# Kernel tuning notes

Hardware: AMD Instinct MI355X
Metric: run time of the kernel (lower is better)

The kernel has to match this reference:

```python
import jax, jax.numpy as jnp
import numpy as np

# Segment geometry (from init_kwargs): modes ['u','uv','v'] -> out_v = alpha * x_u @ W_uv
U = 128
V = 128
IN_OFF = [0, 128, 256, 384]
W_OFF = [k * U * V for k in range(8)]          # [0,16384,...,114688]
OUT_OFF = [0, 128, 256, 384]
IN_STRIDE = 512
OUT_STRIDE = 512
W_STRIDE = 8 * U * V                           # 131072
# (in_seg, w_seg, out_seg, coefficient)
PATHS = [(0, 0, 0, 1.0), (1, 1, 1, 1.0), (2, 2, 2, 1.0), (3, 3, 3, 1.0),
         (0, 4, 1, 0.5), (1, 5, 2, 0.5), (2, 6, 3, 0.5), (3, 7, 0, 0.5)]
B = 32768
E = 4  # num_embeddings (experts)


def setup_inputs() -> dict:
    key = jax.random.key(0)
    k1, k2, k3 = jax.random.split(key, 3)
    tensor_in = jax.random.normal(k1, (B, IN_STRIDE), dtype=jnp.float32)
    tensor_w = jax.random.normal(k2, (E, W_STRIDE), dtype=jnp.float32)
    tensor_w_id = jax.random.randint(k3, (B,), 0, E, dtype=jnp.int32)
    return {"tensor_in": tensor_in, "tensor_w": tensor_w, "tensor_w_id": tensor_w_id}


def _batch_linear(tensor_in, tensor_w, tensor_w_id):
    """Segmented path-indexed grouped linear (cuEquivariance BatchLinear fwd).

    tensor_in: [B, IN_STRIDE]; tensor_w: [E, W_STRIDE]; tensor_w_id: [B] int in [0,E).
    For each path (i, j, k, alpha):
        out[b, OUT_OFF[k]:+V] += alpha * x[b, IN_OFF[i]:+U] @ W[w_id[b], seg j].reshape(U, V)
    """
    nb = tensor_in.shape[0]
    ne = tensor_w.shape[0]
    onehot = jax.nn.one_hot(tensor_w_id, ne, dtype=tensor_in.dtype)  # [B, E]
    out = jnp.zeros((nb, OUT_STRIDE), dtype=tensor_in.dtype)
    for (i, j, k, a) in PATHS:
        x = tensor_in[:, IN_OFF[i]:IN_OFF[i] + U]                    # [B, U]
        w_seg = tensor_w[:, W_OFF[j]:W_OFF[j] + U * V].reshape(ne, U, V)
        # masked per-expert dense GEMMs (small fixed expert count)
        y = jnp.zeros((nb, V), dtype=tensor_in.dtype)
        for e in range(ne):
            y = y + onehot[:, e:e + 1] * (x @ w_seg[e])              # [B, V]
        out = out.at[:, OUT_OFF[k]:OUT_OFF[k] + V].add(a * y)
    return out


def reference(tensor_in, tensor_w, tensor_w_id):
    return _batch_linear(tensor_in, tensor_w, tensor_w_id)
```

## Files before the change

### kernel.cpp

```cpp
#include <hip/hip_runtime.h>
#include <stdint.h>

#define U 128
#define V 128
#define IN_STRIDE 512
#define OUT_STRIDE 512
#define W_STRIDE (8 * U * V)
#define NB 32768
#define NE 4

#define WS_WSHUF 0
#define WS_CNT   1048576
#define WS_SORT  1048640

typedef __bf16 bf16x8 __attribute__((ext_vector_type(8)));
typedef float f32x16 __attribute__((ext_vector_type(16)));
typedef unsigned int u32x4 __attribute__((ext_vector_type(4)));

static __device__ __forceinline__ unsigned short f2bf(float f) {
    unsigned int u = __builtin_bit_cast(unsigned int, f);
    u += 0x7FFFu + ((u >> 16) & 1u);
    return (unsigned short)(u >> 16);
}

__global__ void prep_kernel(const float* __restrict__ w, unsigned short* __restrict__ wshuf,
                            unsigned int* __restrict__ cnt) {
    if (blockIdx.x == 0 && threadIdx.x < NE) cnt[threadIdx.x] = 0u;
    int t = blockIdx.x * 256 + threadIdx.x;
    int lane = t & 63;
    int kt = (t >> 6) & 7;
    int nt = (t >> 9) & 3;
    int s  = (t >> 11) & 7;
    int e  = (t >> 14) & 3;
    int kbase = kt * 16 + ((lane >> 5) << 3);
    int n = nt * 32 + (lane & 31);
    const float* src = w + (size_t)e * W_STRIDE + (size_t)s * (U * V) + n;
    float sc = (s >= 4) ? 0.5f : 1.0f;
    __attribute__((aligned(16))) unsigned short o[8];
#pragma unroll
    for (int j = 0; j < 8; j++) o[j] = f2bf(src[(size_t)(kbase + j) * V] * sc);
    *(u32x4*)(wshuf + (size_t)t * 8) = *(const u32x4*)o;
}

__global__ void scatter_kernel(const int* __restrict__ wid, unsigned int* __restrict__ cnt,
                               int* __restrict__ sorted) {
    __shared__ unsigned int lcnt[NE];
    __shared__ unsigned int lbase[NE];
    int t = threadIdx.x;
    if (t < NE) lcnt[t] = 0u;
    __syncthreads();
    int i = blockIdx.x * 256 + t;
    int e = wid[i];
    unsigned int lpos = atomicAdd(&lcnt[e], 1u);
    __syncthreads();
    if (t < NE) lbase[t] = atomicAdd(&cnt[t], lcnt[t]);
    __syncthreads();
    sorted[e * NB + (int)(lbase[e] + lpos)] = i;
}

__global__ __launch_bounds__(512, 4) void gemm_kernel(
        const float* __restrict__ x, const unsigned short* __restrict__ wshuf,
        const unsigned int* __restrict__ cnt, const int* __restrict__ sorted,
        float* __restrict__ out) {
    const int rowbase = blockIdx.x * 32;
    __shared__ float ldsf[32][512];
    __shared__ int rowid[32];

    const unsigned int p1 = cnt[0];
    const unsigned int p2 = p1 + cnt[1];
    const unsigned int p3 = p2 + cnt[2];

    const int t = threadIdx.x;
    const int w = t >> 6, lane = t & 63;
    const int l5 = lane >> 5, m0 = lane & 31;
    const int kout = w >> 1, nhalf = w & 1;

    int rid[4];
#pragma unroll
    for (int i = 0; i < 4; i++) {
        unsigned int ls = (unsigned int)(rowbase + 4 * w + i);
        int e = (ls >= p1) + (ls >= p2) + (ls >= p3);
        unsigned int pe = (e == 0) ? 0u : (e == 1) ? p1 : (e == 2) ? p2 : p3;
        rid[i] = sorted[e * NB + (int)(ls - pe)];
    }
    if (t < 32) {
        unsigned int ls = (unsigned int)(rowbase + t);
        int e = (ls >= p1) + (ls >= p2) + (ls >= p3);
        unsigned int pe = (e == 0) ? 0u : (e == 1) ? p1 : (e == 2) ? p2 : p3;
        rowid[t] = sorted[e * NB + (int)(ls - pe)];
    }

#pragma unroll
    for (int i = 0; i < 4; i++) {
        int r = 4 * w + i;
        int rs = r & 7;
        const float* xb = x + (size_t)rid[i] * IN_STRIDE + ((m0 ^ rs) << 2) + l5 * 128;
#pragma unroll
        for (int h = 0; h < 2; h++) {
            __builtin_amdgcn_global_load_lds(
                (const __attribute__((address_space(1))) unsigned int*)(xb + h * 256),
                (__attribute__((address_space(3))) unsigned int*)&ldsf[r][h * 256],
                16, 0, 0);
        }
    }

    const unsigned int lh = (unsigned int)rowbase, lt = (unsigned int)(rowbase + 31);
    const int ehead = (lh >= p1) + (lh >= p2) + (lh >= p3);
    const int etail = (lt >= p1) + (lt >= p2) + (lt >= p3);
    const unsigned int l0 = (unsigned int)(rowbase + m0);
    const int e0 = (l0 >= p1) + (l0 >= p2) + (l0 >= p3);

    const int xbc1 = (kout + 3) & 3;
    const int xbs[2] = {kout, xbc1};
    const int sgs[2] = {kout, xbc1 + 4};
    const int rsw = m0 & 7;

    f32x16 acc0 = {}, acc1 = {};

    if (ehead == etail) {
        const unsigned short* wb0 =
            wshuf + (size_t)(((ehead * 8 + sgs[0]) * 4 + nhalf * 2) * 8) * 512 + (size_t)lane * 8;
        u32x4 bp[8];
#pragma unroll
        for (int kt = 0; kt < 4; kt++) {
            bp[kt * 2]     = *(const u32x4*)(wb0 + (size_t)kt * 512);
            bp[kt * 2 + 1] = *(const u32x4*)(wb0 + (size_t)(8 + kt) * 512);
        }
        __syncthreads();

#pragma unroll
        for (int c = 0; c < 2; c++) {
            const float* ar = &ldsf[m0][xbs[c] * 128];
            const unsigned short* wb =
                wshuf + (size_t)(((ehead * 8 + sgs[c]) * 4 + nhalf * 2) * 8) * 512 + (size_t)lane * 8;
#pragma unroll
            for (int kt = 0; kt < 8; kt++) {
                int gj0 = kt * 4 + l5 * 2;
                float4 va = *(const float4*)(ar + ((gj0 ^ rsw) << 2));
                float4 vb = *(const float4*)(ar + (((gj0 + 1) ^ rsw) << 2));
                bf16x8 a;
                a[0] = (__bf16)va.x; a[1] = (__bf16)va.y;
                a[2] = (__bf16)va.z; a[3] = (__bf16)va.w;
                a[4] = (__bf16)vb.x; a[5] = (__bf16)vb.y;
                a[6] = (__bf16)vb.z; a[7] = (__bf16)vb.w;
                bf16x8 b0, b1;
                if (c == 0 && kt < 4) {
                    b0 = __builtin_bit_cast(bf16x8, bp[kt * 2]);
                    b1 = __builtin_bit_cast(bf16x8, bp[kt * 2 + 1]);
                } else {
                    b0 = __builtin_bit_cast(bf16x8, *(const u32x4*)(wb + (size_t)kt * 512));
                    b1 = __builtin_bit_cast(bf16x8, *(const u32x4*)(wb + (size_t)(8 + kt) * 512));
                }
                acc0 = __builtin_amdgcn_mfma_f32_32x32x16_bf16(a, b0, acc0, 0, 0, 0);
                acc1 = __builtin_amdgcn_mfma_f32_32x32x16_bf16(a, b1, acc1, 0, 0, 0);
            }
        }
    } else {
        unsigned int msk[4];
#pragma unroll
        for (int e = 0; e < 4; e++) msk[e] = (e0 == e) ? 0xFFFFFFFFu : 0u;
        __syncthreads();
#pragma unroll
        for (int c = 0; c < 2; c++) {
            const float* ar = &ldsf[m0][xbs[c] * 128];
#pragma unroll
            for (int kt = 0; kt < 8; kt++) {
                int gj0 = kt * 4 + l5 * 2;
                float4 va = *(const float4*)(ar + ((gj0 ^ rsw) << 2));
                float4 vb = *(const float4*)(ar + (((gj0 + 1) ^ rsw) << 2));
                __attribute__((aligned(16))) unsigned short au[8];
                au[0] = f2bf(va.x); au[1] = f2bf(va.y);
                au[2] = f2bf(va.z); au[3] = f2bf(va.w);
                au[4] = f2bf(vb.x); au[5] = f2bf(vb.y);
                au[6] = f2bf(vb.z); au[7] = f2bf(vb.w);
                u32x4 araw = *(const u32x4*)au;
#pragma unroll
                for (int e = 0; e < 4; e++) {
                    u32x4 mm = {msk[e], msk[e], msk[e], msk[e]};
                    bf16x8 am = __builtin_bit_cast(bf16x8, araw & mm);
                    const unsigned short* wb =
                        wshuf + (size_t)(((e * 8 + sgs[c]) * 4 + nhalf * 2) * 8) * 512 + (size_t)lane * 8;
                    bf16x8 b0 = __builtin_bit_cast(bf16x8, *(const u32x4*)(wb + (size_t)kt * 512));
                    bf16x8 b1 = __builtin_bit_cast(bf16x8, *(const u32x4*)(wb + (size_t)(8 + kt) * 512));
                    acc0 = __builtin_amdgcn_mfma_f32_32x32x16_bf16(am, b0, acc0, 0, 0, 0);
                    acc1 = __builtin_amdgcn_mfma_f32_32x32x16_bf16(am, b1, acc1, 0, 0, 0);
                }
            }
        }
    }

    const int colb = kout * 128 + nhalf * 64 + m0;
    const int rh = l5 << 2;
#pragma unroll
    for (int q = 0; q < 4; q++) {
#pragma unroll
        for (int d = 0; d < 4; d++) {
            int reg = q * 4 + d;
            int rl = d + 8 * q + rh;
            float* o = out + (size_t)rowid[rl] * OUT_STRIDE + colb;
            o[0]  = acc0[reg];
            o[32] = acc1[reg];
        }
    }
}

extern "C" void kernel_launch(void* const* d_in, const int* in_sizes, int n_in,
                              void* d_out, int out_size, void* d_ws, size_t ws_size,
                              hipStream_t stream) {
    const float* x = (const float*)d_in[0];
    const float* w = (const float*)d_in[1];
    const int* wid = (const int*)d_in[2];
    float* out = (float*)d_out;

    unsigned short* wshuf = (unsigned short*)((char*)d_ws + WS_WSHUF);
    unsigned int* cnt = (unsigned int*)((char*)d_ws + WS_CNT);
    int* sorted = (int*)((char*)d_ws + WS_SORT);

    prep_kernel<<<256, 256, 0, stream>>>(w, wshuf, cnt);
    scatter_kernel<<<128, 256, 0, stream>>>(wid, cnt, sorted);
    gemm_kernel<<<1024, 512, 0, stream>>>(x, wshuf, cnt, sorted, out);
}
```

Measured before the change: 136.7 us.

## Make GEMM blocks persistent over four row tiles with double-buffered X and register-resident weights

Result: slower. 198.3 us (+45.0%).

```diff
diff --git a/kernel.cpp b/kernel.cpp
--- a/kernel.cpp
+++ b/kernel.cpp
@@ -8,6 +8,7 @@
 #define W_STRIDE (8 * U * V)
 #define NB 32768
 #define NE 4
+#define NT 4
 
 #define WS_WSHUF 0
 #define WS_CNT   1048576
@@ -58,13 +59,13 @@
     sorted[e * NB + (int)(lbase[e] + lpos)] = i;
 }
 
-__global__ __launch_bounds__(512, 4) void gemm_kernel(
+__global__ __launch_bounds__(512, 2) void gemm_kernel(
         const float* __restrict__ x, const unsigned short* __restrict__ wshuf,
         const unsigned int* __restrict__ cnt, const int* __restrict__ sorted,
         float* __restrict__ out) {
-    const int rowbase = blockIdx.x * 32;
-    __shared__ float ldsf[32][512];
-    __shared__ int rowid[32];
+    const int blk = blockIdx.x;
+    __shared__ float ldsf[2][32][512];
+    __shared__ int rowid[128];
 
     const unsigned int p1 = cnt[0];
     const unsigned int p2 = p1 + cnt[1];
@@ -74,134 +75,179 @@
     const int w = t >> 6, lane = t & 63;
     const int l5 = lane >> 5, m0 = lane & 31;
     const int kout = w >> 1, nhalf = w & 1;
-
-    int rid[4];
-#pragma unroll
-    for (int i = 0; i < 4; i++) {
-        unsigned int ls = (unsigned int)(rowbase + 4 * w + i);
-        int e = (ls >= p1) + (ls >= p2) + (ls >= p3);
-        unsigned int pe = (e == 0) ? 0u : (e == 1) ? p1 : (e == 2) ? p2 : p3;
-        rid[i] = sorted[e * NB + (int)(ls - pe)];
+    const int rsw = m0 & 7;
+    const int xb1 = (kout + 3) & 3;
+
+#define EXPERT_OF(ls) (((ls) >= p1) + ((ls) >= p2) + ((ls) >= p3))
+#define PREFIX_OF(e)  ((e) == 0 ? 0u : (e) == 1 ? p1 : (e) == 2 ? p2 : p3)
+
+    if (t < 128) {
+        unsigned int ls = (unsigned int)(blk * 128 + t);
+        int e = EXPERT_OF(ls);
+        rowid[t] = sorted[e * NB + (int)(ls - PREFIX_OF(e))];
     }
-    if (t < 32) {
-        unsigned int ls = (unsigned int)(rowbase + t);
-        int e = (ls >= p1) + (ls >= p2) + (ls >= p3);
-        unsigned int pe = (e == 0) ? 0u : (e == 1) ? p1 : (e == 2) ? p2 : p3;
-        rowid[t] = sorted[e * NB + (int)(ls - pe)];
-    }
+
+    u32x4 bp[32];
+
+#define LOADB(eu) do { \
+    _Pragma("unroll") \
+    for (int c_ = 0; c_ < 2; c_++) { \
+        const int sg_ = c_ ? (xb1 + 4) : kout; \
+        const unsigned short* wb_ = wshuf + \
+            (size_t)((((eu) * 8 + sg_) * 4 + nhalf * 2) * 8) * 512 + (size_t)lane * 8; \
+        _Pragma("unroll") \
+        for (int kt_ = 0; kt_ < 8; kt_++) { \
+            bp[c_ * 16 + kt_ * 2]     = *(const u32x4*)(wb_ + (size_t)kt_ * 512); \
+            bp[c_ * 16 + kt_ * 2 + 1] = *(const u32x4*)(wb_ + (size_t)(8 + kt_) * 512); \
+        } \
+    } \
+} while (0)
+
+#define PINB() do { \
+    asm volatile("" :: "v"(bp[0]),  "v"(bp[1]),  "v"(bp[2]),  "v"(bp[3])); \
+    asm volatile("" :: "v"(bp[4]),  "v"(bp[5]),  "v"(bp[6]),  "v"(bp[7])); \
+    asm volatile("" :: "v"(bp[8]),  "v"(bp[9]),  "v"(bp[10]), "v"(bp[11])); \
+    asm volatile("" :: "v"(bp[12]), "v"(bp[13]), "v"(bp[14]), "v"(bp[15])); \
+    asm volatile("" :: "v"(bp[16]), "v"(bp[17]), "v"(bp[18]), "v"(bp[19])); \
+    asm volatile("" :: "v"(bp[20]), "v"(bp[21]), "v"(bp[22]), "v"(bp[23])); \
+    asm volatile("" :: "v"(bp[24]), "v"(bp[25]), "v"(bp[26]), "v"(bp[27])); \
+    asm volatile("" :: "v"(bp[28]), "v"(bp[29]), "v"(bp[30]), "v"(bp[31])); \
+} while (0)
+
+    const unsigned int rb0 = (unsigned int)(blk * 128);
+    const int e0h = EXPERT_OF(rb0), e0t = EXPERT_OF(rb0 + 31u);
+    int ecur = -1;
+    if (e0h == e0t) { LOADB(e0h); ecur = e0h; PINB(); }
 
 #pragma unroll
     for (int i = 0; i < 4; i++) {
         int r = 4 * w + i;
+        unsigned int ls = (unsigned int)(blk * 128 + r);
+        int e = EXPERT_OF(ls);
+        int rr = sorted[e * NB + (int)(ls - PREFIX_OF(e))];
         int rs = r & 7;
-        const float* xb = x + (size_t)rid[i] * IN_STRIDE + ((m0 ^ rs) << 2) + l5 * 128;
-#pragma unroll
-        for (int h = 0; h < 2; h++) {
-            __builtin_amdgcn_global_load_lds(
-                (const __attribute__((address_space(1))) unsigned int*)(xb + h * 256),
-                (__attribute__((address_space(3))) unsigned int*)&ldsf[r][h * 256],
-                16, 0, 0);
+        const float* xb = x + (size_t)rr * IN_STRIDE + ((m0 ^ rs) << 2) + l5 * 128;
+        __builtin_amdgcn_global_load_lds(
+            (const __attribute__((address_space(1))) unsigned int*)xb,
+            (__attribute__((address_space(3))) unsigned int*)&ldsf[0][r][0], 16, 0, 0);
+        __builtin_amdgcn_global_load_lds(
+            (const __attribute__((address_space(1))) unsigned int*)(xb + 256),
+            (__attribute__((address_space(3))) unsigned int*)&ldsf[0][r][256], 16, 0, 0);
+    }
+
+    asm volatile("s_waitcnt vmcnt(0) lgkmcnt(0)" ::: "memory");
+    __builtin_amdgcn_sched_barrier(0);
+    __builtin_amdgcn_s_barrier();
+    __builtin_amdgcn_sched_barrier(0);
+
+    const int colb = kout * 128 + nhalf * 64 + m0;
+    const int rh = l5 << 2;
+
+    for (int T = 0; T < NT; T++) {
+        const unsigned int rb = (unsigned int)(blk * 128 + T * 32);
+        const int eh = EXPERT_OF(rb), et = EXPERT_OF(rb + 31u);
+        const int fast = (eh == et);
+        const float (*buf)[512] = ldsf[T & 1];
+
+        if (fast && eh != ecur) { LOADB(eh); ecur = eh; PINB(); }
+
+        if (T < NT - 1) {
+#pragma unroll
+            for (int i = 0; i < 4; i++) {
+                int r = 4 * w + i;
+                int rr = rowid[(T + 1) * 32 + r];
+                int rs = r & 7;
+                const float* xb = x + (size_t)rr * IN_STRIDE + ((m0 ^ rs) << 2) + l5 * 128;
+                __builtin_amdgcn_global_load_lds(
+                    (const __attribute__((address_space(1))) unsigned int*)xb,
+                    (__attribute__((address_space(3))) unsigned int*)&ldsf[(T + 1) & 1][r][0], 16, 0, 0);
+                __builtin_amdgcn_global_load_lds(
+                    (const __attribute__((address_space(1))) unsigned int*)(xb + 256),
+                    (__attribute__((address_space(3))) unsigned int*)&ldsf[(T + 1) & 1][r][256], 16, 0, 0);
+            }
+        }
+
+        f32x16 acc0 = {}, acc1 = {};
+
+        if (fast) {
+#pragma unroll
+            for (int c = 0; c < 2; c++) {
+                const float* ar = &buf[m0][(c ? xb1 : kout) * 128];
+#pragma unroll
+                for (int kt = 0; kt < 8; kt++) {
+                    int gj0 = kt * 4 + l5 * 2;
+                    float4 va = *(const float4*)(ar + ((gj0 ^ rsw) << 2));
+                    float4 vb = *(const float4*)(ar + (((gj0 + 1) ^ rsw) << 2));
+                    bf16x8 a;
+                    a[0] = (__bf16)va.x; a[1] = (__bf16)va.y;
+                    a[2] = (__bf16)va.z; a[3] = (__bf16)va.w;
+                    a[4] = (__bf16)vb.x; a[5] = (__bf16)vb.y;
+                    a[6] = (__bf16)vb.z; a[7] = (__bf16)vb.w;
+                    bf16x8 b0 = __builtin_bit_cast(bf16x8, bp[c * 16 + kt * 2]);
+                    bf16x8 b1 = __builtin_bit_cast(bf16x8, bp[c * 16 + kt * 2 + 1]);
+                    acc0 = __builtin_amdgcn_mfma_f32_32x32x16_bf16(a, b0, acc0, 0, 0, 0);
+                    acc1 = __builtin_amdgcn_mfma_f32_32x32x16_bf16(a, b1, acc1, 0, 0, 0);
+                }
+            }
+        } else {
+            const unsigned int l0 = rb + (unsigned int)m0;
+            const int e0 = EXPERT_OF(l0);
+            unsigned int msk[4];
+#pragma unroll
+            for (int e = 0; e < 4; e++) msk[e] = (e0 == e) ? 0xFFFFFFFFu : 0u;
+            const int xbs[2] = {kout, xb1};
+            const int sgs[2] = {kout, xb1 + 4};
+#pragma unroll
+            for (int c = 0; c < 2; c++) {
+                const float* ar = &buf[m0][xbs[c] * 128];
+#pragma unroll
+                for (int kt = 0; kt < 8; kt++) {
+                    int gj0 = kt * 4 + l5 * 2;
+                    float4 va = *(const float4*)(ar + ((gj0 ^ rsw) << 2));
+                    float4 vb = *(const float4*)(ar + (((gj0 + 1) ^ rsw) << 2));
+                    __attribute__((aligned(16))) unsigned short au[8];
+                    au[0] = f2bf(va.x); au[1] = f2bf(va.y);
+                    au[2] = f2bf(va.z); au[3] = f2bf(va.w);
+                    au[4] = f2bf(vb.x); au[5] = f2bf(vb.y);
+                    au[6] = f2bf(vb.z); au[7] = f2bf(vb.w);
+                    u32x4 araw = *(const u32x4*)au;
+#pragma unroll
+                    for (int e = 0; e < 4; e++) {
+                        u32x4 mm = {msk[e], msk[e], msk[e], msk[e]};
+                        bf16x8 am = __builtin_bit_cast(bf16x8, araw & mm);
+                        const unsigned short* wbe = wshuf +
+                            (size_t)(((e * 8 + sgs[c]) * 4 + nhalf * 2) * 8) * 512 + (size_t)lane * 8;
+                        bf16x8 b0 = __builtin_bit_cast(bf16x8, *(const u32x4*)(wbe + (size_t)kt * 512));
+                        bf16x8 b1 = __builtin_bit_cast(bf16x8, *(const u32x4*)(wbe + (size_t)(8 + kt) * 512));
+                        acc0 = __builtin_amdgcn_mfma_f32_32x32x16_bf16(am, b0, acc0, 0, 0, 0);
+                        acc1 = __builtin_amdgcn_mfma_f32_32x32x16_bf16(am, b1, acc1, 0, 0, 0);
+                    }
+                }
+            }
+        }
+
+#pragma unroll
+        for (int q = 0; q < 4; q++)
+#pragma unroll
+            for (int d = 0; d < 4; d++) {
+                int reg = q * 4 + d;
+                int rl = d + 8 * q + rh;
+                float* o = out + (size_t)rowid[T * 32 + rl] * OUT_STRIDE + colb;
+                o[0]  = acc0[reg];
+                o[32] = acc1[reg];
+            }
+
+        if (T < NT - 1) {
+            asm volatile("s_waitcnt vmcnt(32)" ::: "memory");
+            __builtin_amdgcn_sched_barrier(0);
+            __builtin_amdgcn_s_barrier();
+            __builtin_amdgcn_sched_barrier(0);
         }
     }
-
-    const unsigned int lh = (unsigned int)rowbase, lt = (unsigned int)(rowbase + 31);
-    const int ehead = (lh >= p1) + (lh >= p2) + (lh >= p3);
-    const int etail = (lt >= p1) + (lt >= p2) + (lt >= p3);
-    const unsigned int l0 = (unsigned int)(rowbase + m0);
-    const int e0 = (l0 >= p1) + (l0 >= p2) + (l0 >= p3);
-
-    const int xbc1 = (kout + 3) & 3;
-    const int xbs[2] = {kout, xbc1};
-    const int sgs[2] = {kout, xbc1 + 4};
-    const int rsw = m0 & 7;
-
-    f32x16 acc0 = {}, acc1 = {};
-
-    if (ehead == etail) {
-        const unsigned short* wb0 =
-            wshuf + (size_t)(((ehead * 8 + sgs[0]) * 4 + nhalf * 2) * 8) * 512 + (size_t)lane * 8;
-        u32x4 bp[8];
-#pragma unroll
-        for (int kt = 0; kt < 4; kt++) {
-            bp[kt * 2]     = *(const u32x4*)(wb0 + (size_t)kt * 512);
-            bp[kt * 2 + 1] = *(const u32x4*)(wb0 + (size_t)(8 + kt) * 512);
-        }
-        __syncthreads();
-
-#pragma unroll
-        for (int c = 0; c < 2; c++) {
-            const float* ar = &ldsf[m0][xbs[c] * 128];
-            const unsigned short* wb =
-                wshuf + (size_t)(((ehead * 8 + sgs[c]) * 4 + nhalf * 2) * 8) * 512 + (size_t)lane * 8;
-#pragma unroll
-            for (int kt = 0; kt < 8; kt++) {
-                int gj0 = kt * 4 + l5 * 2;
-                float4 va = *(const float4*)(ar + ((gj0 ^ rsw) << 2));
-                float4 vb = *(const float4*)(ar + (((gj0 + 1) ^ rsw) << 2));
-                bf16x8 a;
-                a[0] = (__bf16)va.x; a[1] = (__bf16)va.y;
-                a[2] = (__bf16)va.z; a[3] = (__bf16)va.w;
-                a[4] = (__bf16)vb.x; a[5] = (__bf16)vb.y;
-                a[6] = (__bf16)vb.z; a[7] = (__bf16)vb.w;
-                bf16x8 b0, b1;
-                if (c == 0 && kt < 4) {
-                    b0 = __builtin_bit_cast(bf16x8, bp[kt * 2]);
-                    b1 = __builtin_bit_cast(bf16x8, bp[kt * 2 + 1]);
-                } else {
-                    b0 = __builtin_bit_cast(bf16x8, *(const u32x4*)(wb + (size_t)kt * 512));
-                    b1 = __builtin_bit_cast(bf16x8, *(const u32x4*)(wb + (size_t)(8 + kt) * 512));
-                }
-                acc0 = __builtin_amdgcn_mfma_f32_32x32x16_bf16(a, b0, acc0, 0, 0, 0);
-                acc1 = __builtin_amdgcn_mfma_f32_32x32x16_bf16(a, b1, acc1, 0, 0, 0);
-            }
-        }
-    } else {
-        unsigned int msk[4];
-#pragma unroll
-        for (int e = 0; e < 4; e++) msk[e] = (e0 == e) ? 0xFFFFFFFFu : 0u;
-        __syncthreads();
-#pragma unroll
-        for (int c = 0; c < 2; c++) {
-            const float* ar = &ldsf[m0][xbs[c] * 128];
-#pragma unroll
-            for (int kt = 0; kt < 8; kt++) {
-                int gj0 = kt * 4 + l5 * 2;
-                float4 va = *(const float4*)(ar + ((gj0 ^ rsw) << 2));
-                float4 vb = *(const float4*)(ar + (((gj0 + 1) ^ rsw) << 2));
-                __attribute__((aligned(16))) unsigned short au[8];
-                au[0] = f2bf(va.x); au[1] = f2bf(va.y);
-                au[2] = f2bf(va.z); au[3] = f2bf(va.w);
-                au[4] = f2bf(vb.x); au[5] = f2bf(vb.y);
-                au[6] = f2bf(vb.z); au[7] = f2bf(vb.w);
-                u32x4 araw = *(const u32x4*)au;
-#pragma unroll
-                for (int e = 0; e < 4; e++) {
-                    u32x4 mm = {msk[e], msk[e], msk[e], msk[e]};
-                    bf16x8 am = __builtin_bit_cast(bf16x8, araw & mm);
-                    const unsigned short* wb =
-                        wshuf + (size_t)(((e * 8 + sgs[c]) * 4 + nhalf * 2) * 8) * 512 + (size_t)lane * 8;
-                    bf16x8 b0 = __builtin_bit_cast(bf16x8, *(const u32x4*)(wb + (size_t)kt * 512));
-                    bf16x8 b1 = __builtin_bit_cast(bf16x8, *(const u32x4*)(wb + (size_t)(8 + kt) * 512));
-                    acc0 = __builtin_amdgcn_mfma_f32_32x32x16_bf16(am, b0, acc0, 0, 0, 0);
-                    acc1 = __builtin_amdgcn_mfma_f32_32x32x16_bf16(am, b1, acc1, 0, 0, 0);
-                }
-            }
-        }
-    }
-
-    const int colb = kout * 128 + nhalf * 64 + m0;
-    const int rh = l5 << 2;
-#pragma unroll
-    for (int q = 0; q < 4; q++) {
-#pragma unroll
-        for (int d = 0; d < 4; d++) {
-            int reg = q * 4 + d;
-            int rl = d + 8 * q + rh;
-            float* o = out + (size_t)rowid[rl] * OUT_STRIDE + colb;
-            o[0]  = acc0[reg];
-            o[32] = acc1[reg];
-        }
-    }
+#undef LOADB
+#undef PINB
+#undef EXPERT_OF
+#undef PREFIX_OF
 }
 
 extern "C" void kernel_launch(void* const* d_in, const int* in_sizes, int n_in,
@@ -218,5 +264,5 @@
 
     prep_kernel<<<256, 256, 0, stream>>>(w, wshuf, cnt);
     scatter_kernel<<<128, 256, 0, stream>>>(wid, cnt, sorted);
-    gemm_kernel<<<1024, 512, 0, stream>>>(x, wshuf, cnt, sorted, out);
-}
+    gemm_kernel<<<256, 512, 0, stream>>>(x, wshuf, cnt, sorted, out);
+}
```
